# Performance work log

Hardware: AMD Instinct MI355X
Metric: run time of the kernel (lower is better)

The kernel has to match this reference:

```python
import jax, jax.numpy as jnp
import numpy as np

START_LABEL_ID = 4  # tag_to_ix['[CLS]']


def setup_inputs() -> dict:
    key = jax.random.key(0)
    k1, k2 = jax.random.split(key)
    B, T, K = 256, 4096, 6
    feats = jax.random.normal(k1, (B, T, K), dtype=jnp.float32)
    transitions = jax.random.normal(k2, (B, T, K, K), dtype=jnp.float32)
    return {"feats": feats, "transitions": transitions}


def reference(feats, transitions):
    # Viterbi decode (Bert_BiLSTM_CRF._viterbi_decode):
    #   log_delta init -10000 except start tag; per step t:
    #     scores   = transitions[:, t] + log_delta[:, None, :]   # [B, K, K]
    #     log_delta = max_k scores + feats[:, t]
    #     psi[:, t] = argmax_k scores  (backpointers)
    B, T, K = feats.shape
    init = jnp.full((B, K), -10000.0, dtype=feats.dtype).at[:, START_LABEL_ID].set(0.0)

    def step(delta, xs):
        trans_t, feat_t = xs                       # [B,K,K], [B,K]
        scores = trans_t + delta[:, None, :]       # [B,K,K]
        new_delta = jnp.max(scores, axis=-1) + feat_t
        psi_t = jnp.argmax(scores, axis=-1)        # [B,K] backpointers
        return new_delta, psi_t

    # time-major xs for scan over t = 1..T-1
    xs = (jnp.swapaxes(transitions[:, 1:], 0, 1),  # [T-1,B,K,K]
          jnp.swapaxes(feats[:, 1:], 0, 1))        # [T-1,B,K]
    final_delta, psis = jax.lax.scan(step, init, xs)  # psis: [T-1,B,K]

    score = jnp.max(final_delta, axis=-1)              # [B]
    last_tag = jnp.argmax(final_delta, axis=-1)        # [B]

    # Backtrack: path[t] = psi[t+1][path[t+1]]; psis[i] is psi at time i+1,
    # so path[t] = gather(psis[t], path[t+1]) for t = T-2 .. 0.
    def back(next_tag, psi_t):
        tag = jnp.take_along_axis(psi_t, next_tag[:, None], axis=-1)[:, 0]
        return tag, tag

    _, tags = jax.lax.scan(back, last_tag, psis, reverse=True)  # tags[i] = path[i], i=0..T-2
    path = jnp.concatenate([tags, last_tag[None, :]], axis=0).T  # [B,T]
    return score, path
```

## Files before the change

### kernel.cpp

```cpp
#include <hip/hip_runtime.h>

#define NB 256
#define NT 4096
#define CH 128
#define NCHUNK (NT / CH)

typedef unsigned int u32;
typedef unsigned long long u64;
typedef int v2i __attribute__((ext_vector_type(2)));

typedef __attribute__((address_space(1))) const u32 gas_u32;
typedef __attribute__((address_space(3))) u32 las_u32;

__device__ __forceinline__ void gll16(const void* g, void* l) {
  __builtin_amdgcn_global_load_lds((gas_u32*)g, (las_u32*)l, 16, 0, 0);
}

template <int CTRL>
__device__ __forceinline__ float dppf(float x) {
  return __int_as_float(__builtin_amdgcn_update_dpp(
      0, __float_as_int(x), CTRL, 0xF, 0xF, true));
}

__device__ __forceinline__ float pl16max(float x) {
#if __has_builtin(__builtin_amdgcn_permlane16_swap)
  v2i r = __builtin_amdgcn_permlane16_swap(__float_as_int(x), __float_as_int(x),
                                           false, false);
  return fmaxf(__int_as_float(r[0]), __int_as_float(r[1]));
#else
  return fmaxf(x, __shfl_xor(x, 16, 64));
#endif
}

__device__ __forceinline__ float pl32max(float x) {
#if __has_builtin(__builtin_amdgcn_permlane32_swap)
  v2i r = __builtin_amdgcn_permlane32_swap(__float_as_int(x), __float_as_int(x),
                                           false, false);
  return fmaxf(__int_as_float(r[0]), __int_as_float(r[1]));
#else
  return fmaxf(x, __shfl_xor(x, 32, 64));
#endif
}

__global__ void __launch_bounds__(64, 1)
viterbi_k(const float* __restrict__ feats, const float* __restrict__ trans,
          float* __restrict__ out) {
  __shared__ __align__(16) float s_tr[2 * CH * 36];
  __shared__ __align__(16) float s_ft[2 * CH * 6];
  __shared__ u32 s_psi[NT];
  __shared__ u32 s_path[NT / 4];

  const int b = blockIdx.x;
  const int lane = (int)threadIdx.x;
  const int g = lane >> 3;
  const int l = lane & 7;
  const bool lhi = (l >= 6);
  const bool ghi = (g >= 6);
  const bool sel4 = (lane & 4) != 0;
  const int gg = (g < 6) ? g : 5;
  const int jj = lhi ? 5 : l;
  const int offTA = gg * 6 + jj;
  const int offTB = jj * 6 + gg;
  const int offFA = gg;
  const int offFB = jj;
  const float ninf = __int_as_float(0xff800000u);

  const float* trb = trans + (size_t)b * NT * 36;
  const float* ftb = feats + (size_t)b * NT * 6;

  float delta = (l == 4) ? 0.0f : ((l < 6) ? -10000.0f : ninf);
  u32 mlo = 0, mhi = 0;

  auto stage = [&](int c) {
    const int buf = c & 1;
    const float* gt = trb + (size_t)c * CH * 36;
    float* lt = s_tr + buf * (CH * 36);
#pragma unroll
    for (int i = 0; i < 18; ++i) gll16(gt + i * 256 + lane * 4, lt + i * 256);
    const float* gf = ftb + (size_t)c * CH * 6;
    float* lf = s_ft + buf * (CH * 6);
#pragma unroll
    for (int i = 0; i < 3; ++i) gll16(gf + i * 256 + lane * 4, lf + i * 256);
  };

  auto stepA = [&](float tr, float ft, int slot) {
    float s = tr + delta;
    float m = fmaxf(s, dppf<0xB1>(s));
    m = fmaxf(m, dppf<0x4E>(m));
    float r4 = dppf<0x124>(m);
    float r12 = dppf<0x12C>(m);
    m = fmaxf(m, sel4 ? r4 : r12);
    u64 bal = __ballot(s == m);
    bool cap = (lane == slot);
    mlo = cap ? (u32)bal : mlo;
    mhi = cap ? (u32)(bal >> 32) : mhi;
    delta = m + ft;
  };

  auto stepB = [&](float tr, float ft, int slot) {
    float s = tr + delta;
    float m = fmaxf(s, dppf<0x128>(s));
    m = pl16max(m);
    m = pl32max(m);
    u64 bal = __ballot(s == m);
    bool cap = (lane == slot);
    mlo = cap ? (u32)bal : mlo;
    mhi = cap ? (u32)(bal >> 32) : mhi;
    delta = m + ft;
  };

  auto flush = [&](int base) {
    const u32 ub = (u32)(base >> 6) & 63;
    u32 pA = (u32)__builtin_ctz((mlo & 63u) | 64u);
    pA |= (u32)__builtin_ctz(((mlo >> 8) & 63u) | 64u) << 3;
    pA |= (u32)__builtin_ctz(((mlo >> 16) & 63u) | 64u) << 6;
    pA |= (u32)__builtin_ctz(((mlo >> 24) & 63u) | 64u) << 9;
    pA |= (u32)__builtin_ctz((mhi & 63u) | 64u) << 12;
    pA |= (u32)__builtin_ctz(((mhi >> 8) & 63u) | 64u) << 15;
    u64 bal = ((u64)mhi << 32) | (u64)mlo;
    u32 pB = 0;
#pragma unroll
    for (int i = 0; i < 6; ++i) {
      u64 mm = (bal >> i) & 0x0000010101010101ULL;
      u32 j = (u32)(__builtin_ctzll(mm | (1ULL << 48)) >> 3);
      pB |= j << (3 * i);
    }
    u32 p = (lane & 1) ? pA : pB;
    s_psi[base + (((u32)lane) ^ ub)] = p;
  };

#define LOAD8(trv, ftv, g8base)                                               \
  {                                                                           \
    _Pragma("unroll") for (int q = 0; q < 8; ++q) {                           \
      trv[q] = trp[((g8base) + q) * 36 + ((q & 1) ? offTA : offTB)];          \
      ftv[q] = ftp[((g8base) + q) * 6 + ((q & 1) ? offFA : offFB)];           \
    }                                                                         \
  }

#define STEPS8(trv, ftv, base)                                                \
  {                                                                           \
    _Pragma("unroll") for (int q = 0; q < 8; ++q) {                           \
      if (q & 1) stepA(lhi ? ninf : trv[q], ftv[q], ((base) + q) & 63);       \
      else       stepB(ghi ? ninf : trv[q], ftv[q], ((base) + q) & 63);       \
    }                                                                         \
  }

  stage(0);
  asm volatile("s_waitcnt vmcnt(0)" ::: "memory");
  stage(1);

  {
    const float* trp = s_tr;
    const float* ftp = s_ft;
    float trA[8], ftA[8], trB[8], ftB[8];
    LOAD8(trA, ftA, 0);
    LOAD8(trB, ftB, 8);
#pragma unroll
    for (int q = 1; q < 8; ++q) {
      if (q & 1) stepA(lhi ? ninf : trA[q], ftA[q], q);
      else       stepB(ghi ? ninf : trA[q], ftA[q], q);
    }
    LOAD8(trA, ftA, 16);
    STEPS8(trB, ftB, 8);
#pragma unroll 1
    for (int g2 = 2; g2 < 16; g2 += 2) {
      LOAD8(trB, ftB, (g2 + 1) * 8);
      STEPS8(trA, ftA, g2 * 8);
      LOAD8(trA, ftA, (g2 + 2) * 8);
      STEPS8(trB, ftB, (g2 + 1) * 8);
      if ((g2 & 7) == 6) flush((g2 & 8) * 8);
    }
  }

#pragma unroll 1
  for (int c = 1; c < NCHUNK; ++c) {
    asm volatile("s_waitcnt vmcnt(0)" ::: "memory");
    if (c + 1 < NCHUNK) stage(c + 1);
    const int buf = c & 1;
    const float* trp = s_tr + buf * (CH * 36);
    const float* ftp = s_ft + buf * (CH * 6);
    const int tbase = c * CH;
    float trA[8], ftA[8], trB[8], ftB[8];
    LOAD8(trA, ftA, 0);
#pragma unroll 1
    for (int g2 = 0; g2 < 16; g2 += 2) {
      LOAD8(trB, ftB, (g2 + 1) * 8);
      STEPS8(trA, ftA, tbase + g2 * 8);
      LOAD8(trA, ftA, (g2 + 2) * 8);
      STEPS8(trB, ftB, tbase + (g2 + 1) * 8);
      if ((g2 & 7) == 6) flush(tbase + (g2 & 8) * 8);
    }
  }

  float sm = delta;
  sm = fmaxf(sm, dppf<0xB1>(sm));
  sm = fmaxf(sm, dppf<0x4E>(sm));
  {
    float q4 = dppf<0x124>(sm), q12 = dppf<0x12C>(sm);
    sm = fmaxf(sm, sel4 ? q4 : q12);
  }
  sm = fmaxf(sm, dppf<0x128>(sm));
  sm = pl16max(sm);
  sm = pl32max(sm);
  u64 bs = __ballot(delta == sm);
  int last_tag = (int)((__builtin_ctzll(bs) >> 3) & 7);

  __syncthreads();

  const int u = lane;
  u32 Gm = 0u | (1u << 3) | (2u << 6) | (3u << 9) | (4u << 12) | (5u << 15);
#pragma unroll 1
  for (int k = 0; k < 64; ++k) {
    u32 p = s_psi[u * 64 + (k ^ u)];
    u32 ng = 0;
#pragma unroll
    for (int x = 0; x < 6; ++x) {
      u32 j = (p >> (3 * x)) & 7;
      u32 v = (Gm >> (3 * ((j < 6) ? j : 0))) & 7;
      ng |= v << (3 * x);
    }
    Gm = ng;
  }

  int bcur = last_tag;
  int my_b = last_tag;
#pragma unroll 1
  for (int v = 63; v >= 1; --v) {
    u32 Gv = (u32)__builtin_amdgcn_readlane((int)Gm, v);
    bcur = (int)((Gv >> (3 * bcur)) & 7);
    my_b = (u == v - 1) ? bcur : my_b;
  }

  {
    int tag = my_b;
    unsigned char* pb = (unsigned char*)s_path;
    pb[u * 64 + 63] = (unsigned char)tag;
#pragma unroll 1
    for (int k = 63; k >= 1; --k) {
      u32 p = s_psi[u * 64 + (k ^ u)];
      tag = (int)((p >> (3 * tag)) & 7);
      pb[u * 64 + k - 1] = (unsigned char)tag;
    }
  }
  if (lane == 0) out[b] = sm;
  __syncthreads();

  float* outp = out + NB + (size_t)b * NT;
#pragma unroll
  for (int i = 0; i < (NT / 4) / 64; ++i) {
    u32 w = s_path[lane + i * 64];
    float4 f;
    f.x = (float)(w & 255u);
    f.y = (float)((w >> 8) & 255u);
    f.z = (float)((w >> 16) & 255u);
    f.w = (float)((w >> 24) & 255u);
    ((float4*)outp)[lane + i * 64] = f;
  }
}

extern "C" void kernel_launch(void* const* d_in, const int* in_sizes, int n_in,
                              void* d_out, int out_size, void* d_ws, size_t ws_size,
                              hipStream_t stream) {
  (void)in_sizes; (void)n_in; (void)out_size; (void)d_ws; (void)ws_size;
  const float* feats = (const float*)d_in[0];
  const float* trans = (const float*)d_in[1];
  float* out = (float*)d_out;
  hipLaunchKernelGGL(viterbi_k, dim3(NB), dim3(64), 0, stream, feats, trans, out);
}
```

Baseline: 251.3 us.

## Load inputs directly to registers with 4-deep prefetch, drop LDS staging

Removes the double-buffered global-to-LDS staging of transitions and feats and instead loads each 8-step group straight from global memory into registers, keeping four groups in flight ahead of the serial Viterbi recurrence. It also replaces the two-DPP select in the 8-lane max with a single row_half_mirror DPP and flushes backpointers every 64 steps. The intent is to cut LDS traffic and the waitcnt stalls on the serial dependency chain. The trade-off is many small strided global loads whose latency must be hidden by a prefetch window of only about 32 steps.

```diff
diff --git a/kernel.cpp b/kernel.cpp
--- a/kernel.cpp
+++ b/kernel.cpp
@@ -2,19 +2,10 @@
 
 #define NB 256
 #define NT 4096
-#define CH 128
-#define NCHUNK (NT / CH)
 
 typedef unsigned int u32;
 typedef unsigned long long u64;
 typedef int v2i __attribute__((ext_vector_type(2)));
-
-typedef __attribute__((address_space(1))) const u32 gas_u32;
-typedef __attribute__((address_space(3))) u32 las_u32;
-
-__device__ __forceinline__ void gll16(const void* g, void* l) {
-  __builtin_amdgcn_global_load_lds((gas_u32*)g, (las_u32*)l, 16, 0, 0);
-}
 
 template <int CTRL>
 __device__ __forceinline__ float dppf(float x) {
@@ -45,8 +36,6 @@
 __global__ void __launch_bounds__(64, 1)
 viterbi_k(const float* __restrict__ feats, const float* __restrict__ trans,
           float* __restrict__ out) {
-  __shared__ __align__(16) float s_tr[2 * CH * 36];
-  __shared__ __align__(16) float s_ft[2 * CH * 6];
   __shared__ u32 s_psi[NT];
   __shared__ u32 s_path[NT / 4];
 
@@ -56,7 +45,6 @@
   const int l = lane & 7;
   const bool lhi = (l >= 6);
   const bool ghi = (g >= 6);
-  const bool sel4 = (lane & 4) != 0;
   const int gg = (g < 6) ? g : 5;
   const int jj = lhi ? 5 : l;
   const int offTA = gg * 6 + jj;
@@ -71,25 +59,11 @@
   float delta = (l == 4) ? 0.0f : ((l < 6) ? -10000.0f : ninf);
   u32 mlo = 0, mhi = 0;
 
-  auto stage = [&](int c) {
-    const int buf = c & 1;
-    const float* gt = trb + (size_t)c * CH * 36;
-    float* lt = s_tr + buf * (CH * 36);
-#pragma unroll
-    for (int i = 0; i < 18; ++i) gll16(gt + i * 256 + lane * 4, lt + i * 256);
-    const float* gf = ftb + (size_t)c * CH * 6;
-    float* lf = s_ft + buf * (CH * 6);
-#pragma unroll
-    for (int i = 0; i < 3; ++i) gll16(gf + i * 256 + lane * 4, lf + i * 256);
-  };
-
   auto stepA = [&](float tr, float ft, int slot) {
     float s = tr + delta;
     float m = fmaxf(s, dppf<0xB1>(s));
     m = fmaxf(m, dppf<0x4E>(m));
-    float r4 = dppf<0x124>(m);
-    float r12 = dppf<0x12C>(m);
-    m = fmaxf(m, sel4 ? r4 : r12);
+    m = fmaxf(m, dppf<0x141>(m));
     u64 bal = __ballot(s == m);
     bool cap = (lane == slot);
     mlo = cap ? (u32)bal : mlo;
@@ -129,76 +103,66 @@
     s_psi[base + (((u32)lane) ^ ub)] = p;
   };
 
-#define LOAD8(trv, ftv, g8base)                                               \
+#define LOADG(TRV, FTV, GID)                                                  \
+  {                                                                           \
+    int g8 = (GID) * 8;                                                       \
+    if (g8 > NT - 8) g8 = NT - 8;   \
+    const float* trg = trb + (size_t)g8 * 36;                                 \
+    const float* ftg = ftb + (size_t)g8 * 6;                                  \
+    _Pragma("unroll") for (int q = 0; q < 8; ++q) {                           \
+      TRV[q] = trg[q * 36 + ((q & 1) ? offTA : offTB)];                       \
+      FTV[q] = ftg[q * 6 + ((q & 1) ? offFA : offFB)];                        \
+    }                                                                         \
+  }
+
+#define STEPS8(TRV, FTV, B8)                                                  \
   {                                                                           \
     _Pragma("unroll") for (int q = 0; q < 8; ++q) {                           \
-      trv[q] = trp[((g8base) + q) * 36 + ((q & 1) ? offTA : offTB)];          \
-      ftv[q] = ftp[((g8base) + q) * 6 + ((q & 1) ? offFA : offFB)];           \
+      if (q & 1) stepA(lhi ? ninf : TRV[q], FTV[q], (B8) + q);                \
+      else       stepB(ghi ? ninf : TRV[q], FTV[q], (B8) + q);                \
     }                                                                         \
   }
 
-#define STEPS8(trv, ftv, base)                                                \
-  {                                                                           \
-    _Pragma("unroll") for (int q = 0; q < 8; ++q) {                           \
-      if (q & 1) stepA(lhi ? ninf : trv[q], ftv[q], ((base) + q) & 63);       \
-      else       stepB(ghi ? ninf : trv[q], ftv[q], ((base) + q) & 63);       \
-    }                                                                         \
-  }
-
-  stage(0);
-  asm volatile("s_waitcnt vmcnt(0)" ::: "memory");
-  stage(1);
-
-  {
-    const float* trp = s_tr;
-    const float* ftp = s_ft;
-    float trA[8], ftA[8], trB[8], ftB[8];
-    LOAD8(trA, ftA, 0);
-    LOAD8(trB, ftB, 8);
-#pragma unroll
-    for (int q = 1; q < 8; ++q) {
-      if (q & 1) stepA(lhi ? ninf : trA[q], ftA[q], q);
-      else       stepB(ghi ? ninf : trA[q], ftA[q], q);
-    }
-    LOAD8(trA, ftA, 16);
-    STEPS8(trB, ftB, 8);
-#pragma unroll 1
-    for (int g2 = 2; g2 < 16; g2 += 2) {
-      LOAD8(trB, ftB, (g2 + 1) * 8);
-      STEPS8(trA, ftA, g2 * 8);
-      LOAD8(trA, ftA, (g2 + 2) * 8);
-      STEPS8(trB, ftB, (g2 + 1) * 8);
-      if ((g2 & 7) == 6) flush((g2 & 8) * 8);
-    }
-  }
-
-#pragma unroll 1
-  for (int c = 1; c < NCHUNK; ++c) {
-    asm volatile("s_waitcnt vmcnt(0)" ::: "memory");
-    if (c + 1 < NCHUNK) stage(c + 1);
-    const int buf = c & 1;
-    const float* trp = s_tr + buf * (CH * 36);
-    const float* ftp = s_ft + buf * (CH * 6);
-    const int tbase = c * CH;
-    float trA[8], ftA[8], trB[8], ftB[8];
-    LOAD8(trA, ftA, 0);
-#pragma unroll 1
-    for (int g2 = 0; g2 < 16; g2 += 2) {
-      LOAD8(trB, ftB, (g2 + 1) * 8);
-      STEPS8(trA, ftA, tbase + g2 * 8);
-      LOAD8(trA, ftA, (g2 + 2) * 8);
-      STEPS8(trB, ftB, tbase + (g2 + 1) * 8);
-      if ((g2 & 7) == 6) flush(tbase + (g2 & 8) * 8);
-    }
+  float tr0[8], ft0[8], tr1[8], ft1[8], tr2[8], ft2[8], tr3[8], ft3[8];
+  LOADG(tr0, ft0, 0)
+  LOADG(tr1, ft1, 1)
+  LOADG(tr2, ft2, 2)
+  LOADG(tr3, ft3, 3)
+
+#pragma unroll 1
+  for (int w = 0; w < NT / 64; ++w) {
+    const int gbase = w * 8;
+    if (w == 0) {
+#pragma unroll
+      for (int q = 1; q < 8; ++q) {
+        if (q & 1) stepA(lhi ? ninf : tr0[q], ft0[q], q);
+        else       stepB(ghi ? ninf : tr0[q], ft0[q], q);
+      }
+    } else {
+      STEPS8(tr0, ft0, 0)
+    }
+    LOADG(tr0, ft0, gbase + 4)
+    STEPS8(tr1, ft1, 8)
+    LOADG(tr1, ft1, gbase + 5)
+    STEPS8(tr2, ft2, 16)
+    LOADG(tr2, ft2, gbase + 6)
+    STEPS8(tr3, ft3, 24)
+    LOADG(tr3, ft3, gbase + 7)
+    STEPS8(tr0, ft0, 32)
+    LOADG(tr0, ft0, gbase + 8)
+    STEPS8(tr1, ft1, 40)
+    LOADG(tr1, ft1, gbase + 9)
+    STEPS8(tr2, ft2, 48)
+    LOADG(tr2, ft2, gbase + 10)
+    STEPS8(tr3, ft3, 56)
+    LOADG(tr3, ft3, gbase + 11)
+    flush(w * 64);
   }
 
   float sm = delta;
   sm = fmaxf(sm, dppf<0xB1>(sm));
   sm = fmaxf(sm, dppf<0x4E>(sm));
-  {
-    float q4 = dppf<0x124>(sm), q12 = dppf<0x12C>(sm);
-    sm = fmaxf(sm, sel4 ? q4 : q12);
-  }
+  sm = fmaxf(sm, dppf<0x141>(sm));
   sm = fmaxf(sm, dppf<0x128>(sm));
   sm = pl16max(sm);
   sm = pl32max(sm);
```

Result: slower. 708.7 us (+182.0%).
